# Kernel optimization log

Hardware: AMD Instinct MI355X
Metric: run time of the kernel (lower is better)

## Reference

```python
import jax, jax.numpy as jnp
from jax import lax
import numpy as np

K = 3          # kernelsize
RX = RY = 3.0  # dilated_rates * kernelsize
BN_EPS = 1e-3  # keras BatchNormalization default


def setup_inputs() -> dict:
    key = jax.random.key(0)
    k1, k2, k3 = jax.random.split(key, 3)
    B, H, W, C, F = 8, 128, 128, 64, 64
    return {
        "fmap": jax.random.normal(k1, (B, H, W, C), jnp.float32),
        "y2": jax.random.normal(k2, (B, H, W, 8), jnp.float32),
        "conv_w": jax.random.normal(k3, (K, K, C, F), jnp.float32) * np.sqrt(2.0 / (K * K * C)),
        "gamma": jnp.ones((F,), jnp.float32),
        "beta": jnp.zeros((F,), jnp.float32),
        "moving_mean": jnp.zeros((F,), jnp.float32),
        "moving_var": jnp.ones((F,), jnp.float32),
    }


def reference(fmap, y2, conv_w, gamma, beta, moving_mean, moving_var):
    B, H, W, C = fmap.shape
    HW = H * W
    N = HW * K * K

    xs = jnp.clip(jnp.flip(jnp.sort(y2[..., 0:4], axis=-1), -1)[..., 0:2], 1.0, W - 1)  # [B,H,W,2]
    ys = jnp.clip(jnp.flip(jnp.sort(y2[..., 4:8], axis=-1), -1)[..., 0:2], 1.0, H - 1)
    w = jnp.sum(xs, axis=-1, keepdims=True)  # [B,H,W,1]
    h = jnp.sum(ys, axis=-1, keepdims=True)

    # base pixel grids flattened as in the TF code: row[i*W+j]=i, column[i*W+j]=j
    row = jnp.repeat(jnp.arange(H, dtype=jnp.float32), W).reshape(HW, 1)
    column = jnp.tile(jnp.arange(W, dtype=jnp.float32), H).reshape(HW, 1)

    wf = (w / RX).reshape(B, HW, 1)
    w0 = (w * 1e-10).reshape(B, HW, 1)
    x_samp = jnp.concatenate([column - 1.0 - wf, column + w0, column + 1.0 + wf], axis=-1)  # [B,HW,3]
    x_samp = jnp.tile(x_samp.reshape(-1, H, W, 1), (1, 1, 1, K))  # [3B,H,W,3] (same layout as TF)

    hf = (h / RY).reshape(B, HW, 1)
    h0 = (h * 1e-10).reshape(B, HW, 1)
    y_samp = jnp.concatenate([row - 1.0 - hf, row + h0, row + 1.0 + hf], axis=-1)
    y_samp = jnp.tile(y_samp.reshape(-1, H, W, 1), (1, 1, 1, K))  # [3B,H,W,3]

    x_left = jnp.clip(jnp.floor(x_samp), 0.0, W - 1)
    x_right = jnp.clip(jnp.ceil(x_samp), 0.0, W - 1)
    y_top = jnp.clip(jnp.floor(y_samp), 0.0, H - 1)
    y_bottom = jnp.clip(jnp.ceil(y_samp), 0.0, H - 1)

    def flat(a):  # -> [B, N, 1] (broadcast over C replaces TF's tile)
        return a.reshape(-1, N)[:, :, None]

    xr_x = flat(x_right - x_samp)
    xl_x = flat(x_samp - x_left)
    yt_y = flat(y_samp - y_top)
    yb_y = flat(y_bottom - y_samp)

    idx_lt = (y_top * W + x_left).reshape(-1, N).astype(jnp.int32)
    idx_rt = (y_top * W + x_right).reshape(-1, N).astype(jnp.int32)
    idx_lb = (y_bottom * W + x_left).reshape(-1, N).astype(jnp.int32)
    idx_rb = (y_bottom * W + x_right).reshape(-1, N).astype(jnp.int32)

    fmap2 = fmap.reshape(B, HW, C)
    gather = lambda idx: jnp.take_along_axis(fmap2, idx[:, :, None], axis=1)  # [B,N,C]

    f_lt, f_rt = gather(idx_lt), gather(idx_rt)
    f_lb, f_rb = gather(idx_lb), gather(idx_rb)

    f = (xr_x * f_lt + xl_x * f_lb) * yb_y + (xr_x * f_rt + xl_x * f_rb) * yt_y  # [B,N,C]
    f = f.reshape(-1, H * K, W * K, C)  # [B, 3H, 3W, C]

    out = lax.conv_general_dilated(
        f, conv_w, window_strides=(K, K), padding="VALID",
        dimension_numbers=("NHWC", "HWIO", "NHWC"))  # [B,H,W,F]

    out = (out - moving_mean) * (gamma / jnp.sqrt(moving_var + BN_EPS)) + beta
    return jax.nn.relu(out)
```

## Files before the change

### kernel.cpp

```cpp
#include <hip/hip_runtime.h>

typedef __bf16 bf16x8 __attribute__((ext_vector_type(8)));
typedef float f32x4 __attribute__((ext_vector_type(4)));

__device__ __forceinline__ unsigned short f2bf(float f) {
  __bf16 h = (__bf16)f;
  return __builtin_bit_cast(unsigned short, h);
}

__global__ __launch_bounds__(256) void prep_kernel(
    const float* __restrict__ conv_w, const float* __restrict__ gamma,
    const float* __restrict__ beta, const float* __restrict__ mean,
    const float* __restrict__ var, unsigned short* __restrict__ wsB,
    float* __restrict__ bias) {
  int idx = blockIdx.x * 256 + threadIdx.x;
  if (idx >= 12288) return;
  int di    = idx >> 12;
  int r     = idx & 4095;
  int jblk  = r >> 10;
  int r2    = r & 1023;
  int kstep = r2 >> 9;
  int r3    = r2 & 511;
  int lane  = r3 >> 3;
  int i     = r3 & 7;
  int c   = kstep * 32 + 4 * (lane >> 4) + (i & 3) + 16 * (i >> 2);
  int fch = jblk * 16 + (lane & 15);
  float s = gamma[fch] * rsqrtf(var[fch] + 1e-3f);
  float v = conv_w[((di * 3 + 0) * 64 + c) * 64 + fch]
          + conv_w[((di * 3 + 1) * 64 + c) * 64 + fch]
          + conv_w[((di * 3 + 2) * 64 + c) * 64 + fch];
  wsB[idx] = f2bf(v * s);
  if (idx < 64) bias[idx] = beta[idx] - mean[idx] * (gamma[idx] * rsqrtf(var[idx] + 1e-3f));
}

__global__ __launch_bounds__(256, 4) void main_kernel(
    const float* __restrict__ fmap, const float* __restrict__ y2,
    const uint4* __restrict__ wsBq, const float* __restrict__ biasg,
    float* __restrict__ out) {
  __shared__ int   s_idx[4][384];
  __shared__ float s_wt[4][384];
  __shared__ uint2 fsA[4][4][64][2];

  const int t    = threadIdx.x;
  const int lane = t & 63;
  const int wave = t >> 6;
  const int b  = blockIdx.x & 7;
  const int oi = blockIdx.x >> 3;
  const float* fmapb = fmap + (size_t)b * (128 * 128 * 64);

  #pragma unroll
  for (int it = 0; it < 2; ++it) {
    int e = lane + 64 * it;
    if (e < 96) {
      int di  = e >> 5;
      int upl = e & 31;
      int up  = wave * 32 + upl;
      int u   = di * 128 + up;
      int j   = u / 3;
      int a   = u - j * 3;
      const float4* yp = reinterpret_cast<const float4*>(
          y2 + ((size_t)(b * 128 + oi) * 128 + j) * 8);
      float4 xv = yp[0];
      float4 yv = yp[1];

      float hi01 = fmaxf(xv.x, xv.y), lo01 = fminf(xv.x, xv.y);
      float hi23 = fmaxf(xv.z, xv.w), lo23 = fminf(xv.z, xv.w);
      float top1 = fmaxf(hi01, hi23);
      float top2 = fmaxf(fminf(hi01, hi23), (hi01 >= hi23) ? lo01 : lo23);
      float w = fminf(fmaxf(top1, 1.f), 127.f) + fminf(fmaxf(top2, 1.f), 127.f);

      hi01 = fmaxf(yv.x, yv.y); lo01 = fminf(yv.x, yv.y);
      hi23 = fmaxf(yv.z, yv.w); lo23 = fminf(yv.z, yv.w);
      top1 = fmaxf(hi01, hi23);
      top2 = fmaxf(fminf(hi01, hi23), (hi01 >= hi23) ? lo01 : lo23);
      float h = fminf(fmaxf(top1, 1.f), 127.f) + fminf(fmaxf(top2, 1.f), 127.f);

      float x, yy;
      if (a == 0)      { x = ((float)j - 1.0f) - w / 3.0f;  yy = ((float)oi - 1.0f) - h / 3.0f; }
      else if (a == 1) { x = (float)j + w * 1e-10f;         yy = (float)oi + h * 1e-10f; }
      else             { x = ((float)j + 1.0f) + w / 3.0f;  yy = ((float)oi + 1.0f) + h / 3.0f; }

      float xl = fminf(fmaxf(floorf(x), 0.f), 127.f);
      float xr = fminf(fmaxf(ceilf(x),  0.f), 127.f);
      float yt = fminf(fmaxf(floorf(yy), 0.f), 127.f);
      float yb = fminf(fmaxf(ceilf(yy),  0.f), 127.f);
      int ixl = (int)xl, ixr = (int)xr, iyt = (int)yt, iyb = (int)yb;
      s_idx[0][u] = (iyt * 128 + ixl) * 64;
      s_idx[1][u] = (iyt * 128 + ixr) * 64;
      s_idx[2][u] = (iyb * 128 + ixl) * 64;
      s_idx[3][u] = (iyb * 128 + ixr) * 64;
      s_wt[0][u] = xr - x;
      s_wt[1][u] = x - xl;
      s_wt[2][u] = yy - yt;
      s_wt[3][u] = yb - yy;
    }
  }
  __builtin_amdgcn_wave_barrier();

  const int px15 = lane & 15;
  float bias4[4];
  #pragma unroll
  for (int j = 0; j < 4; ++j) bias4[j] = biasg[j * 16 + px15];

  f32x4 acc[2][4];
  #pragma unroll
  for (int p = 0; p < 2; ++p)
    #pragma unroll
    for (int j = 0; j < 4; ++j)
      acc[p][j] = (f32x4){bias4[j], bias4[j], bias4[j], bias4[j]};

  const int cg    = lane & 15;
  const int g     = cg & 3;
  const int hh    = (cg >> 2) & 1;
  const int kstepS= cg >> 3;
  const int upg   = lane >> 4;
  const int lsr   = lane ^ (2 * (lane >> 4));

  for (int di = 0; di < 3; ++di) {
    bf16x8 Bf[8];
    #pragma unroll
    for (int jk = 0; jk < 8; ++jk)
      Bf[jk] = __builtin_bit_cast(bf16x8, wsBq[(di * 8 + jk) * 64 + lane]);

    #pragma unroll 4
    for (int r = 0; r < 8; ++r) {
      int upl = r * 4 + upg;
      int up  = wave * 32 + upl;
      int u   = di * 128 + up;
      float xr_x = s_wt[0][u], xl_x = s_wt[1][u];
      float yt_y = s_wt[2][u], yb_y = s_wt[3][u];
      bool need = ((xr_x != 0.f) || (xl_x != 0.f)) &&
                  ((yb_y != 0.f) || (yt_y != 0.f));
      uint2 q = make_uint2(0u, 0u);
      if (need) {
        int c0 = cg * 4;
        int i0 = s_idx[0][u], i1 = s_idx[1][u];
        int i2 = s_idx[2][u], i3 = s_idx[3][u];
        float4 lt = *reinterpret_cast<const float4*>(fmapb + i0 + c0);
        float4 rt = *reinterpret_cast<const float4*>(fmapb + i1 + c0);
        float4 lb = *reinterpret_cast<const float4*>(fmapb + i2 + c0);
        float4 rb = *reinterpret_cast<const float4*>(fmapb + i3 + c0);
        float v0 = (xr_x * lt.x + xl_x * lb.x) * yb_y + (xr_x * rt.x + xl_x * rb.x) * yt_y;
        float v1 = (xr_x * lt.y + xl_x * lb.y) * yb_y + (xr_x * rt.y + xl_x * rb.y) * yt_y;
        float v2 = (xr_x * lt.z + xl_x * lb.z) * yb_y + (xr_x * rt.z + xl_x * rb.z) * yt_y;
        float v3 = (xr_x * lt.w + xl_x * lb.w) * yb_y + (xr_x * rt.w + xl_x * rb.w) * yt_y;
        q.x = (unsigned)f2bf(v0) | ((unsigned)f2bf(v1) << 16);
        q.y = (unsigned)f2bf(v2) | ((unsigned)f2bf(v3) << 16);
      }
      int lpp = ((upl & 15) | (g << 4)) ^ (g << 1);
      fsA[wave][(upl >> 4) * 2 + kstepS][lpp][hh] = q;
    }
    __builtin_amdgcn_wave_barrier();

    #pragma unroll
    for (int kstep = 0; kstep < 2; ++kstep) {
      #pragma unroll
      for (int p = 0; p < 2; ++p) {
        bf16x8 a = __builtin_bit_cast(bf16x8,
            *reinterpret_cast<const uint4*>(&fsA[wave][p * 2 + kstep][lsr][0]));
        #pragma unroll
        for (int j = 0; j < 4; ++j)
          acc[p][j] = __builtin_amdgcn_mfma_f32_16x16x32_bf16(a, Bf[j * 2 + kstep],
                                                              acc[p][j], 0, 0, 0);
      }
    }
    __builtin_amdgcn_wave_barrier();
  }

  float* outb = out + ((size_t)(b * 128 + oi) * 128) * 64;
  #pragma unroll
  for (int p = 0; p < 2; ++p) {
    int pxB = (wave * 2 + p) * 16 + (lane >> 4) * 4;
    #pragma unroll
    for (int j = 0; j < 4; ++j) {
      int fch = j * 16 + px15;
      #pragma unroll
      for (int reg = 0; reg < 4; ++reg) {
        outb[(size_t)(pxB + reg) * 64 + fch] = fmaxf(acc[p][j][reg], 0.f);
      }
    }
  }
}

extern "C" void kernel_launch(void* const* d_in, const int* in_sizes, int n_in,
                              void* d_out, int out_size, void* d_ws, size_t ws_size,
                              hipStream_t stream) {
  const float* fmap   = (const float*)d_in[0];
  const float* y2     = (const float*)d_in[1];
  const float* conv_w = (const float*)d_in[2];
  const float* gamma  = (const float*)d_in[3];
  const float* beta   = (const float*)d_in[4];
  const float* mean   = (const float*)d_in[5];
  const float* var    = (const float*)d_in[6];
  float* outp = (float*)d_out;

  unsigned short* wsB = (unsigned short*)d_ws;
  float* bias = (float*)((char*)d_ws + 24576);

  prep_kernel<<<48, 256, 0, stream>>>(conv_w, gamma, beta, mean, var, wsB, bias);
  main_kernel<<<1024, 256, 0, stream>>>(fmap, y2, (const uint4*)d_ws, bias, outp);
}
```

Before: 32.21 us.

## Software-pipeline bilinear gathers two steps ahead and pack LDS tables as vec4

The gather/interpolate loop is flattened across all three kernel rows into a 24-step fully unrolled loop. Each step issues the four global fmap loads for a sample two steps ahead while it interpolates the current one, hiding gather latency behind compute. The per-sample index and weight tables in shared memory are stored as int4/float4, so each sample needs one LDS read instead of four. This raises register pressure, with two in-flight sets of five float4 values, which could limit occupancy under the launch bounds of 256 threads and 4 blocks.

Result: slower. 46.52 us (+44.4%).

```diff
diff --git a/kernel.cpp b/kernel.cpp
--- a/kernel.cpp
+++ b/kernel.cpp
@@ -37,9 +37,9 @@
     const float* __restrict__ fmap, const float* __restrict__ y2,
     const uint4* __restrict__ wsBq, const float* __restrict__ biasg,
     float* __restrict__ out) {
-  __shared__ int   s_idx[4][384];
-  __shared__ float s_wt[4][384];
-  __shared__ uint2 fsA[4][4][64][2];
+  __shared__ int4   s_idx4[384];
+  __shared__ float4 s_wt4[384];
+  __shared__ uint2  fsA[4][4][64][2];
 
   const int t    = threadIdx.x;
   const int lane = t & 63;
@@ -85,87 +85,103 @@
       float yt = fminf(fmaxf(floorf(yy), 0.f), 127.f);
       float yb = fminf(fmaxf(ceilf(yy),  0.f), 127.f);
       int ixl = (int)xl, ixr = (int)xr, iyt = (int)yt, iyb = (int)yb;
-      s_idx[0][u] = (iyt * 128 + ixl) * 64;
-      s_idx[1][u] = (iyt * 128 + ixr) * 64;
-      s_idx[2][u] = (iyb * 128 + ixl) * 64;
-      s_idx[3][u] = (iyb * 128 + ixr) * 64;
-      s_wt[0][u] = xr - x;
-      s_wt[1][u] = x - xl;
-      s_wt[2][u] = yy - yt;
-      s_wt[3][u] = yb - yy;
+      s_idx4[u] = make_int4((iyt * 128 + ixl) * 64, (iyt * 128 + ixr) * 64,
+                            (iyb * 128 + ixl) * 64, (iyb * 128 + ixr) * 64);
+      s_wt4[u]  = make_float4(xr - x, x - xl, yy - yt, yb - yy);
     }
   }
   __builtin_amdgcn_wave_barrier();
 
   const int px15 = lane & 15;
-  float bias4[4];
-  #pragma unroll
-  for (int j = 0; j < 4; ++j) bias4[j] = biasg[j * 16 + px15];
+  const int cg   = lane & 15;
+  const int g    = cg & 3;
+  const int hh   = (cg >> 2) & 1;
+  const int ksS  = cg >> 3;
+  const int upg  = lane >> 4;
+  const int lsr  = lane ^ (2 * (lane >> 4));
+  const int c0   = cg * 4;
 
   f32x4 acc[2][4];
   #pragma unroll
-  for (int p = 0; p < 2; ++p)
-    #pragma unroll
-    for (int j = 0; j < 4; ++j)
-      acc[p][j] = (f32x4){bias4[j], bias4[j], bias4[j], bias4[j]};
-
-  const int cg    = lane & 15;
-  const int g     = cg & 3;
-  const int hh    = (cg >> 2) & 1;
-  const int kstepS= cg >> 3;
-  const int upg   = lane >> 4;
-  const int lsr   = lane ^ (2 * (lane >> 4));
-
-  for (int di = 0; di < 3; ++di) {
-    bf16x8 Bf[8];
-    #pragma unroll
-    for (int jk = 0; jk < 8; ++jk)
-      Bf[jk] = __builtin_bit_cast(bf16x8, wsBq[(di * 8 + jk) * 64 + lane]);
-
-    #pragma unroll 4
-    for (int r = 0; r < 8; ++r) {
-      int upl = r * 4 + upg;
-      int up  = wave * 32 + upl;
-      int u   = di * 128 + up;
-      float xr_x = s_wt[0][u], xl_x = s_wt[1][u];
-      float yt_y = s_wt[2][u], yb_y = s_wt[3][u];
-      bool need = ((xr_x != 0.f) || (xl_x != 0.f)) &&
-                  ((yb_y != 0.f) || (yt_y != 0.f));
-      uint2 q = make_uint2(0u, 0u);
-      if (need) {
-        int c0 = cg * 4;
-        int i0 = s_idx[0][u], i1 = s_idx[1][u];
-        int i2 = s_idx[2][u], i3 = s_idx[3][u];
-        float4 lt = *reinterpret_cast<const float4*>(fmapb + i0 + c0);
-        float4 rt = *reinterpret_cast<const float4*>(fmapb + i1 + c0);
-        float4 lb = *reinterpret_cast<const float4*>(fmapb + i2 + c0);
-        float4 rb = *reinterpret_cast<const float4*>(fmapb + i3 + c0);
-        float v0 = (xr_x * lt.x + xl_x * lb.x) * yb_y + (xr_x * rt.x + xl_x * rb.x) * yt_y;
-        float v1 = (xr_x * lt.y + xl_x * lb.y) * yb_y + (xr_x * rt.y + xl_x * rb.y) * yt_y;
-        float v2 = (xr_x * lt.z + xl_x * lb.z) * yb_y + (xr_x * rt.z + xl_x * rb.z) * yt_y;
-        float v3 = (xr_x * lt.w + xl_x * lb.w) * yb_y + (xr_x * rt.w + xl_x * rb.w) * yt_y;
-        q.x = (unsigned)f2bf(v0) | ((unsigned)f2bf(v1) << 16);
-        q.y = (unsigned)f2bf(v2) | ((unsigned)f2bf(v3) << 16);
+  for (int j = 0; j < 4; ++j) {
+    float bv = biasg[j * 16 + px15];
+    acc[0][j] = (f32x4){bv, bv, bv, bv};
+    acc[1][j] = (f32x4){bv, bv, bv, bv};
+  }
+
+  bf16x8 Bf[8];
+
+  float4 lt_A, rt_A, lb_A, rb_A, Wt_A;
+  float4 lt_B, rt_B, lb_B, rb_B, Wt_B;
+  lt_A = rt_A = lb_A = rb_A = Wt_A = make_float4(0.f, 0.f, 0.f, 0.f);
+  lt_B = rt_B = lb_B = rb_B = Wt_B = make_float4(0.f, 0.f, 0.f, 0.f);
+
+#define ISSUE(mm, S) {                                                        \
+    const int u_ = ((mm) >> 3) * 128 + wave * 32 + ((mm) & 7) * 4 + upg;      \
+    Wt_##S = s_wt4[u_];                                                       \
+    bool need_ = ((Wt_##S.x != 0.f) || (Wt_##S.y != 0.f)) &&                  \
+                 ((Wt_##S.w != 0.f) || (Wt_##S.z != 0.f));                    \
+    if (need_) {                                                              \
+      int4 I_ = s_idx4[u_];                                                   \
+      lt_##S = *reinterpret_cast<const float4*>(fmapb + I_.x + c0);           \
+      rt_##S = *reinterpret_cast<const float4*>(fmapb + I_.y + c0);           \
+      lb_##S = *reinterpret_cast<const float4*>(fmapb + I_.z + c0);           \
+      rb_##S = *reinterpret_cast<const float4*>(fmapb + I_.w + c0);           \
+    }                                                                         \
+  }
+
+#define CONSUME(mm, S) {                                                      \
+    const int pxi_ = ((mm) & 7) * 4 + upg;                                    \
+    bool need_ = ((Wt_##S.x != 0.f) || (Wt_##S.y != 0.f)) &&                  \
+                 ((Wt_##S.w != 0.f) || (Wt_##S.z != 0.f));                    \
+    uint2 q_ = make_uint2(0u, 0u);                                            \
+    if (need_) {                                                              \
+      float xr_x = Wt_##S.x, xl_x = Wt_##S.y, yt_y = Wt_##S.z, yb_y = Wt_##S.w; \
+      float v0 = (xr_x * lt_##S.x + xl_x * lb_##S.x) * yb_y + (xr_x * rt_##S.x + xl_x * rb_##S.x) * yt_y; \
+      float v1 = (xr_x * lt_##S.y + xl_x * lb_##S.y) * yb_y + (xr_x * rt_##S.y + xl_x * rb_##S.y) * yt_y; \
+      float v2 = (xr_x * lt_##S.z + xl_x * lb_##S.z) * yb_y + (xr_x * rt_##S.z + xl_x * rb_##S.z) * yt_y; \
+      float v3 = (xr_x * lt_##S.w + xl_x * lb_##S.w) * yb_y + (xr_x * rt_##S.w + xl_x * rb_##S.w) * yt_y; \
+      q_.x = (unsigned)f2bf(v0) | ((unsigned)f2bf(v1) << 16);                 \
+      q_.y = (unsigned)f2bf(v2) | ((unsigned)f2bf(v3) << 16);                 \
+    }                                                                         \
+    int lpp_ = ((pxi_ & 15) | (g << 4)) ^ (g << 1);                           \
+    fsA[wave][(pxi_ >> 4) * 2 + ksS][lpp_][hh] = q_;                          \
+  }
+
+  ISSUE(0, A);
+  ISSUE(1, B);
+
+  #pragma unroll
+  for (int m = 0; m < 24; ++m) {
+    if ((m & 7) == 0) {
+      const int di_ = m >> 3;
+      #pragma unroll
+      for (int jk = 0; jk < 8; ++jk)
+        Bf[jk] = __builtin_bit_cast(bf16x8, wsBq[(di_ * 8 + jk) * 64 + lane]);
+    }
+    if ((m & 1) == 0) { CONSUME(m, A); } else { CONSUME(m, B); }
+    if (m < 22) {
+      if ((m & 1) == 0) { ISSUE(m + 2, A); } else { ISSUE(m + 2, B); }
+    }
+    if ((m & 7) == 7) {
+      __builtin_amdgcn_wave_barrier();
+      #pragma unroll
+      for (int ks = 0; ks < 2; ++ks) {
+        #pragma unroll
+        for (int p = 0; p < 2; ++p) {
+          bf16x8 a = __builtin_bit_cast(bf16x8,
+              *reinterpret_cast<const uint4*>(&fsA[wave][p * 2 + ks][lsr][0]));
+          #pragma unroll
+          for (int j = 0; j < 4; ++j)
+            acc[p][j] = __builtin_amdgcn_mfma_f32_16x16x32_bf16(a, Bf[j * 2 + ks],
+                                                                acc[p][j], 0, 0, 0);
+        }
       }
-      int lpp = ((upl & 15) | (g << 4)) ^ (g << 1);
-      fsA[wave][(upl >> 4) * 2 + kstepS][lpp][hh] = q;
-    }
-    __builtin_amdgcn_wave_barrier();
-
-    #pragma unroll
-    for (int kstep = 0; kstep < 2; ++kstep) {
-      #pragma unroll
-      for (int p = 0; p < 2; ++p) {
-        bf16x8 a = __builtin_bit_cast(bf16x8,
-            *reinterpret_cast<const uint4*>(&fsA[wave][p * 2 + kstep][lsr][0]));
-        #pragma unroll
-        for (int j = 0; j < 4; ++j)
-          acc[p][j] = __builtin_amdgcn_mfma_f32_16x16x32_bf16(a, Bf[j * 2 + kstep],
-                                                              acc[p][j], 0, 0, 0);
-      }
-    }
-    __builtin_amdgcn_wave_barrier();
-  }
+      __builtin_amdgcn_wave_barrier();
+    }
+  }
+#undef ISSUE
+#undef CONSUME
 
   float* outb = out + ((size_t)(b * 128 + oi) * 128) * 64;
   #pragma unroll
```
